# Kernel tuning notes

Measured on AMD Instinct MI355X. Metric: run time of the kernel, lower is better.

The kernel has to match this reference:

```python
import jax, jax.numpy as jnp
import numpy as np

WH, WW = 12, 12
NUM_HEADS = 8
NW = 4


def _relative_position_index():
    ch, cw = np.meshgrid(np.arange(WH), np.arange(WW), indexing='ij')
    coords = np.stack([ch, cw]).reshape(2, -1)            # [2, Wh*Ww]
    rel = coords[:, :, None] - coords[:, None, :]         # [2, M, M]
    rel = rel.transpose(1, 2, 0)                          # [M, M, 2]
    rel[:, :, 0] += WH - 1
    rel[:, :, 1] += WW - 1
    rel[:, :, 0] *= 2 * WW - 1
    return jnp.asarray(rel.sum(-1))                       # [M, M] int


def setup_inputs() -> dict:
    key = jax.random.key(0)
    ks = jax.random.split(key, 11)
    C = 512
    B_, N = 512, WH * WW + 1
    std = 0.02
    return {
        'x': jax.random.normal(ks[0], (B_, N, C), dtype=jnp.float32),
        'mask': jnp.zeros((NW, N, N), dtype=jnp.float32),
        'rpb_table': jax.random.normal(ks[1], ((2 * WH - 1) * (2 * WW - 1), NUM_HEADS), dtype=jnp.float32) * std,
        'Wq': jax.random.normal(ks[2], (C, C), dtype=jnp.float32) * (C ** -0.5),
        'bq': jax.random.normal(ks[3], (C,), dtype=jnp.float32) * std,
        'Wk': jax.random.normal(ks[4], (C, C), dtype=jnp.float32) * (C ** -0.5),
        'bk': jax.random.normal(ks[5], (C,), dtype=jnp.float32) * std,
        'Wv': jax.random.normal(ks[6], (C, C), dtype=jnp.float32) * (C ** -0.5),
        'bv': jax.random.normal(ks[7], (C,), dtype=jnp.float32) * std,
        'Wo': jax.random.normal(ks[8], (C, C), dtype=jnp.float32) * (C ** -0.5),
        'bo': jax.random.normal(ks[9], (C,), dtype=jnp.float32) * std,
    }


def reference(x, mask, rpb_table, Wq, bq, Wk, bk, Wv, bv, Wo, bo):
    B_, N, C = x.shape
    H = NUM_HEADS
    hd = C // H
    scale = hd ** -0.5
    B = B_ // NW
    M = WH * WW  # window tokens (N = M + 1 global token)

    def proj(W, b):
        return (x @ W.T + b).reshape(B_, N, H, hd).transpose(0, 2, 1, 3)  # [B_,H,N,hd]

    q = proj(Wq, bq)
    k = proj(Wk, bk)
    v = proj(Wv, bv)

    attn = jnp.einsum('bhnd,bhmd->bhnm', q, k) * scale  # [B_,H,N,N]

    rel_idx = _relative_position_index()                 # [M,M]
    bias = rpb_table[rel_idx].transpose(2, 0, 1)          # [H,M,M]
    attn = attn.at[:, :, :M, :M].add(bias[None])          # N != M: bias on window block only

    # shifted-window mask: (nW, N, N)
    attn = (attn.reshape(B, NW, H, N, N) + mask[None, :, None]).reshape(B_, H, N, N)

    # ---- global-token attention redistribution (gx) ----
    ga = attn[:, :, -1, :].reshape(B, NW, H, N).transpose(0, 2, 1, 3)   # [B,H,NW,N]
    g1 = ga[:, :, :, :M].reshape(B, H, NW * M)                           # window keys, all windows
    g2 = ga[:, :, :, M].mean(-1, keepdims=True)                          # mean global-global logit [B,H,1]
    g = jax.nn.softmax(jnp.concatenate([g1, g2], axis=-1), axis=-1)      # [B,H,NW*M+1]
    g1 = g[:, :, :-1].reshape(B, H, NW, M).transpose(0, 2, 1, 3).reshape(B_, H, M)
    g2 = jnp.broadcast_to(g[:, :, -1][:, None, :], (B, NW, H)).reshape(B_, H, 1)
    ga_full = jnp.concatenate([g1, g2], axis=-1)[:, :, None, :]          # [B_,H,1,N]
    gx = jnp.einsum('bhqn,bhnd->bhqd', ga_full, v).transpose(0, 2, 1, 3).reshape(B_, C)
    gx = gx.reshape(B, NW, C).sum(1)                                     # sum over windows [B,C]
    gx = jnp.broadcast_to(gx[:, None, :], (B, NW, C)).reshape(B_, C)

    # ---- standard window attention ----
    attn = jax.nn.softmax(attn, axis=-1)
    out = jnp.einsum('bhnm,bhmd->bhnd', attn, v).transpose(0, 2, 1, 3).reshape(B_, N, C)
    out = out.at[:, -1, :].set(gx)
    return out @ Wo.T + bo
```

## Files before the change

kernel.cpp:

```cpp
#include <hip/hip_runtime.h>
#include <hip/hip_bf16.h>
#include <stdint.h>

#define NTOK 145
#define MTOK 144
#define CDIM 512
#define NHEAD 8
#define HD 64
#define NWIN 4
#define BWIN 512
#define MROWS (BWIN*NTOK)

typedef short short8 __attribute__((ext_vector_type(8)));
typedef float f32x4 __attribute__((ext_vector_type(4)));

__device__ __forceinline__ uint16_t f2bf(float f) {
  union { float f; uint32_t u; } x; x.f = f;
  uint32_t r = x.u + 0x7FFFu + ((x.u >> 16) & 1u);
  return (uint16_t)(r >> 16);
}
__device__ __forceinline__ float bf2f(uint16_t u) {
  union { uint32_t u; float f; } x; x.u = ((uint32_t)u) << 16; return x.f;
}
__device__ __forceinline__ uint32_t pack2(float a, float b) {
  return (uint32_t)f2bf(a) | ((uint32_t)f2bf(b) << 16);
}

#define GLL(gp, lp) __builtin_amdgcn_global_load_lds( \
    (const __attribute__((address_space(1))) uint32_t*)(gp), \
    (__attribute__((address_space(3))) uint32_t*)(lp), 16, 0, 0)

__global__ __launch_bounds__(256) void cast_x(const float* __restrict__ x,
                                              uint16_t* __restrict__ xb) {
  size_t id = ((size_t)blockIdx.x*256 + threadIdx.x)*8;
  float4 a = *(const float4*)(x+id), c = *(const float4*)(x+id+4);
  uint4 o = make_uint4(pack2(a.x,a.y), pack2(a.z,a.w), pack2(c.x,c.y), pack2(c.z,c.w));
  *(uint4*)(xb+id) = o;
}

__global__ void prep_kernel(const float* __restrict__ rpb,
                            const float* __restrict__ Wq, const float* __restrict__ bq,
                            const float* __restrict__ Wk, const float* __restrict__ bk,
                            const float* __restrict__ Wv, const float* __restrict__ bv,
                            const float* __restrict__ Wo, const float* __restrict__ mask,
                            uint16_t* __restrict__ wqkv, uint16_t* __restrict__ wo,
                            float* __restrict__ bqkv, float* __restrict__ ltab) {
  int id = blockIdx.x * 256 + threadIdx.x;
  const int A = 1536*512, B = 512*512, C2 = 1536, E = 4*8*145*160;
  if (id < A) {
    int n = id >> 9, k = id & 511;
    const float* W = (n < 512) ? Wq : (n < 1024) ? Wk : Wv;
    wqkv[id] = f2bf(W[(size_t)(n & 511)*512 + k]);
  } else if ((id -= A) < B) {
    wo[id] = f2bf(Wo[id]);
  } else if ((id -= B) < C2) {
    bqkv[id] = (id < 512) ? bq[id] : (id < 1024) ? bk[id-512] : bv[id-1024];
  } else if ((id -= C2) < E) {
    int nw = id / (8*145*160);
    int r2 = id % (8*145*160);
    int h = r2 / (145*160);
    int r3 = r2 % (145*160);
    int i = r3 / 160, j = r3 % 160;
    float v = 0.f;
    if (j < 145) v = mask[(nw*145 + i)*145 + j];
    if (i < 144 && j < 144) {
      int rel = (i/12 - j/12 + 11) * 23 + (i%12 - j%12 + 11);
      v += rpb[rel*8 + h];
    }
    ltab[id] = v;
  }
}

__global__ __launch_bounds__(512, 2) void gemm_qkv(
    const uint16_t* __restrict__ xb, const uint16_t* __restrict__ wqkv,
    const float* __restrict__ bqkv,
    uint16_t* __restrict__ qb, uint16_t* __restrict__ kb, uint16_t* __restrict__ vb) {
  __shared__ __align__(16) uint16_t As[4*256*32];
  __shared__ __align__(16) uint16_t Bs[4*256*32];
  int bid = blockIdx.x;
  int mb, nb;
  if (bid < 1728) { int g = bid / 48, r = bid % 48; mb = g*8 + (r & 7); nb = r >> 3; }
  else            { int r = bid - 1728;             mb = 288 + (r & 1); nb = r >> 1; }
  int tid = threadIdx.x, lane = tid & 63, w = tid >> 6;
  int wnA = w >> 2;
  int wmB = w & 3;
  int lm = lane & 15, lq = lane >> 4;

  int srow = lane >> 2;
  int schunk = (lane & 3) ^ ((lane >> 3) & 3);
  const uint16_t* agp = xb   + (size_t)(mb*256 + w*32 + srow)*512 + schunk*8;
  const uint16_t* bgp = wqkv + (size_t)(nb*256 + w*32 + srow)*512 + schunk*8;
  int rc = (lq ^ ((lm >> 1) & 3)) * 8;

  f32x4 acc[8][4];
#pragma unroll
  for (int a = 0; a < 8; a++)
#pragma unroll
    for (int b = 0; b < 4; b++) acc[a][b] = (f32x4){0.f,0.f,0.f,0.f};

  #define STAGE_QKV(slot, kt) { \
    uint16_t* Ad = &As[(slot)*8192 + (w*32)*32]; \
    uint16_t* Bd = &Bs[(slot)*8192 + (w*32)*32]; \
    GLL(agp + (kt)*32,           Ad); \
    GLL(agp + (kt)*32 + 16*512,  Ad + 16*32); \
    GLL(bgp + (kt)*32,           Bd); \
    GLL(bgp + (kt)*32 + 16*512,  Bd + 16*32); \
  }

  #define COMPUTE_QKV(slot) { \
    const uint16_t* Wb = &Bs[(slot)*8192 + (wnA*128 + lm)*32 + rc]; \
    const uint16_t* Xb = &As[(slot)*8192 + (wmB*64  + lm)*32 + rc]; \
    short8 wf[8], xf[4]; \
    _Pragma("unroll") \
    for (int na = 0; na < 8; na++) wf[na] = *(const short8*)&Wb[na*16*32]; \
    _Pragma("unroll") \
    for (int mt = 0; mt < 4; mt++) xf[mt] = *(const short8*)&Xb[mt*16*32]; \
    __builtin_amdgcn_s_setprio(1); \
    _Pragma("unroll") \
    for (int na = 0; na < 8; na++) \
      _Pragma("unroll") \
      for (int mt = 0; mt < 4; mt++) \
        acc[na][mt] = __builtin_amdgcn_mfma_f32_16x16x32_bf16(wf[na], xf[mt], acc[na][mt], 0, 0, 0); \
    __builtin_amdgcn_s_setprio(0); \
  }

  STAGE_QKV(0, 0);
  STAGE_QKV(1, 1);
  for (int kt = 0; kt < 15; kt++) {
    asm volatile("s_waitcnt vmcnt(4)" ::: "memory");
    __builtin_amdgcn_s_barrier();
    __builtin_amdgcn_sched_barrier(0);
    if (kt < 14) STAGE_QKV((kt + 2) & 3, kt + 2);
    COMPUTE_QKV(kt & 3);
  }
  asm volatile("s_waitcnt vmcnt(0)" ::: "memory");
  __builtin_amdgcn_s_barrier();
  __builtin_amdgcn_sched_barrier(0);
  COMPUTE_QKV(3);

  #undef STAGE_QKV
  #undef COMPUTE_QKV

  int which = nb >> 1;
  uint16_t* dst = (which == 0) ? qb : (which == 1) ? kb : vb;
#pragma unroll
  for (int mt = 0; mt < 4; mt++) {
    int m = mb*256 + wmB*64 + mt*16 + lm;
    int bw = m / 145, nl = m - bw*145;
    size_t mbase = (size_t)bw*8*9280 + (size_t)nl*64;
#pragma unroll
    for (int na = 0; na < 8; na++) {
      int n0 = nb*256 + wnA*128 + na*16 + lq*4;
      float4 b4 = *(const float4*)&bqkv[n0];
      int c = n0 & 511;
      int hh = c >> 6, d0 = c & 63;
      float f0 = acc[na][mt][0] + b4.x;
      float f1 = acc[na][mt][1] + b4.y;
      float f2 = acc[na][mt][2] + b4.z;
      float f3 = acc[na][mt][3] + b4.w;
      uint32_t lo, hi;
      asm("v_cvt_pk_bf16_f32 %0, %1, %2" : "=v"(lo) : "v"(f0), "v"(f1));
      asm("v_cvt_pk_bf16_f32 %0, %1, %2" : "=v"(hi) : "v"(f2), "v"(f3));
      uint2 pk; pk.x = lo; pk.y = hi;
      *(uint2*)(dst + mbase + (size_t)hh*9280 + d0) = pk;
    }
  }
}

__global__ __launch_bounds__(256, 3) void attn_kernel(
    const uint16_t* __restrict__ qb, const uint16_t* __restrict__ kb,
    const uint16_t* __restrict__ vb, const float* __restrict__ ltab,
    float* __restrict__ glog, uint16_t* __restrict__ attn_out) {
  __shared__ __align__(16) uint16_t P[80*168];
  __shared__ __align__(16) uint16_t vt[64*168];
  int bid = blockIdx.x;
  int half = bid & 1;
  int h = (bid >> 1) & 7;
  int b_ = bid >> 4;
  int nw = b_ & 3;
  int tid = threadIdx.x, lane = tid & 63, w = tid >> 6;
  int lm = lane & 15, lq = lane >> 4;
  const size_t hbase = ((size_t)(b_*8 + h)) * (145*64);
  const uint16_t* qp = qb + hbase;
  const uint16_t* kp = kb + hbase;
  const uint16_t* vp = vb + hbase;
  const float* ltp = ltab + (size_t)(nw*8 + h)*(145*160);

  for (int c = tid; c < 1160; c += 256) {
    int j = c >> 3, d0 = (c & 7) * 8;
    uint16_t tmp[8];
    *(uint4*)tmp = *(const uint4*)(vp + (size_t)j*64 + d0);
#pragma unroll
    for (int t = 0; t < 8; t++) vt[(d0 + t)*168 + j] = tmp[t];
  }
  for (int c = tid; c < 960; c += 256)
    vt[(c/15)*168 + 145 + (c%15)] = 0;

  for (int ltile = w; ltile < 5; ltile += 4) {
    int gt = half*5 + ltile;
    f32x4 acc[10];
#pragma unroll
    for (int nt = 0; nt < 10; nt++) {
#pragma unroll
      for (int r = 0; r < 4; r++) {
        int i = gt*16 + lq*4 + r; if (i > 144) i = 144;
        acc[nt][r] = 8.0f * ltp[i*160 + nt*16 + lm];
      }
    }
    int iq = gt*16 + lm; if (iq > 144) iq = 144;
#pragma unroll
    for (int ks = 0; ks < 2; ks++) {
      short8 afr = *(const short8*)(qp + (size_t)iq*64 + ks*32 + lq*8);
#pragma unroll
      for (int nt = 0; nt < 10; nt++) {
        int j = nt*16 + lm; if (j > 144) j = 144;
        short8 bfr = *(const short8*)(kp + (size_t)j*64 + ks*32 + lq*8);
        acc[nt] = __builtin_amdgcn_mfma_f32_16x16x32_bf16(afr, bfr, acc[nt], 0, 0, 0);
      }
    }
    if (gt == 9) {
      if (lq == 0) {
#pragma unroll
        for (int nt = 0; nt < 10; nt++) {
          int j = nt*16 + lm;
          if (j < 145)
            glog[(size_t)(b_*8 + h)*145 + j] = acc[nt][0]*0.125f;
        }
      }
    } else {
#pragma unroll
      for (int r = 0; r < 4; r++) {
        int prow = ltile*16 + lq*4 + r;
        float mx = -3.0e38f;
#pragma unroll
        for (int nt = 0; nt < 10; nt++) {
          int j = nt*16 + lm;
          float t = acc[nt][r]*0.125f;
          if (j >= 145) t = -3.0e38f;
          acc[nt][r] = t;
          mx = fmaxf(mx, t);
        }
#pragma unroll
        for (int off = 1; off < 16; off <<= 1) mx = fmaxf(mx, __shfl_xor(mx, off));
        float sum = 0.f;
#pragma unroll
        for (int nt = 0; nt < 10; nt++) {
          int j = nt*16 + lm;
          float p = (j < 145) ? __expf(acc[nt][r] - mx) : 0.f;
          acc[nt][r] = p; sum += p;
        }
#pragma unroll
        for (int off = 1; off < 16; off <<= 1) sum += __shfl_xor(sum, off);
        float rs = __builtin_amdgcn_rcpf(sum);
#pragma unroll
        for (int nt = 0; nt < 10; nt++)
          P[prow*168 + nt*16 + lm] = f2bf(acc[nt][r] * rs);
      }
    }
  }
  __syncthreads();

  int npv = 5 - half;
  f32x4 oacc[5];
#pragma unroll
  for (int mt = 0; mt < 5; mt++) oacc[mt] = (f32x4){0.f,0.f,0.f,0.f};
#pragma unroll
  for (int ks = 0; ks < 5; ks++) {
    short8 bfr = *(const short8*)&vt[(w*16 + lm)*168 + ks*32 + lq*8];
#pragma unroll
    for (int mt = 0; mt < 5; mt++) {
      if (mt < npv) {
        short8 afr = *(const short8*)&P[(mt*16 + lm)*168 + ks*32 + lq*8];
        oacc[mt] = __builtin_amdgcn_mfma_f32_16x16x32_bf16(afr, bfr, oacc[mt], 0, 0, 0);
      }
    }
  }
#pragma unroll
  for (int mt = 0; mt < 5; mt++) {
    if (mt < npv) {
#pragma unroll
      for (int r = 0; r < 4; r++) {
        int i = half*80 + mt*16 + lq*4 + r;
        attn_out[((size_t)b_*145 + i)*512 + h*64 + w*16 + lm] = f2bf(oacc[mt][r]);
      }
    }
  }
}

__global__ __launch_bounds__(256) void gx_kernel(
    const float* __restrict__ glog, const uint16_t* __restrict__ vb,
    uint16_t* __restrict__ attn_out) {
  int bid = blockIdx.x;
  int b = bid >> 3, h = bid & 7;
  int tid = threadIdx.x, lane = tid & 63, w = tid >> 6;
  __shared__ float lg[580];
  __shared__ float pl[576];
  __shared__ float sred[8];
  __shared__ float sacc[256];
  for (int t = tid; t < 580; t += 256) {
    int nwi = t / 145, j = t - nwi*145;
    lg[t] = glog[(size_t)((b*4 + nwi)*8 + h)*145 + j];
  }
  __syncthreads();
  float g2 = 0.25f*(lg[144] + lg[289] + lg[434] + lg[579]);
  float mx = g2;
  for (int t = tid; t < 576; t += 256) {
    int nwi = t / 144, j = t - nwi*144;
    mx = fmaxf(mx, lg[nwi*145 + j]);
  }
#pragma unroll
  for (int off = 1; off < 64; off <<= 1) mx = fmaxf(mx, __shfl_xor(mx, off));
  if (lane == 0) sred[w] = mx;
  __syncthreads();
  mx = fmaxf(fmaxf(sred[0], sred[1]), fmaxf(sred[2], sred[3]));
  float sum = 0.f;
  for (int t = tid; t < 576; t += 256) {
    int nwi = t / 144, j = t - nwi*144;
    float p = __expf(lg[nwi*145 + j] - mx);
    pl[t] = p; sum += p;
  }
#pragma unroll
  for (int off = 1; off < 64; off <<= 1) sum += __shfl_xor(sum, off);
  if (lane == 0) sred[4 + w] = sum;
  __syncthreads();
  sum = (sred[4] + sred[5]) + (sred[6] + sred[7]);
  float p2 = __expf(g2 - mx);
  float rs = __builtin_amdgcn_rcpf(sum + p2);
  const uint16_t* vp = vb + (size_t)((b*4 + w)*8 + h)*(145*64);
  float acc = 0.f;
  int d = lane;
#pragma unroll 4
  for (int j = 0; j < 144; j++)
    acc += pl[w*144 + j] * bf2f(vp[j*64 + d]);
  acc += p2 * bf2f(vp[144*64 + d]);
  sacc[tid] = acc;
  __syncthreads();
  if (w == 0) {
    float tot = (sacc[lane] + sacc[64 + lane]) + (sacc[128 + lane] + sacc[192 + lane]);
    uint16_t o = f2bf(tot * rs);
    for (int nwi = 0; nwi < 4; nwi++)
      attn_out[((size_t)(b*4 + nwi)*145 + 144)*512 + h*64 + d] = o;
  }
}

__global__ __launch_bounds__(512, 2) void gemm_out(
    const uint16_t* __restrict__ A, const uint16_t* __restrict__ wo,
    const float* __restrict__ bo, float* __restrict__ out) {
  __shared__ __align__(16) uint16_t As[4*256*32];
  __shared__ __align__(16) uint16_t Bs[4*256*32];
  int bid = blockIdx.x;
  int mb, nb;
  if (bid < 576) { int g = bid / 16, r = bid % 16; mb = g*8 + (r & 7); nb = r >> 3; }
  else           { int r = bid - 576;              mb = 288 + (r & 1); nb = r >> 1; }
  int tid = threadIdx.x, lane = tid & 63, w = tid >> 6;
  int wnA = w >> 2;
  int wmB = w & 3;
  int lm = lane & 15, lq = lane >> 4;

  int srow = lane >> 2;
  int schunk = (lane & 3) ^ ((lane >> 3) & 3);
  const uint16_t* agp = A  + (size_t)(mb*256 + w*32 + srow)*512 + schunk*8;
  const uint16_t* bgp = wo + (size_t)(nb*256 + w*32 + srow)*512 + schunk*8;
  int rc = (lq ^ ((lm >> 1) & 3)) * 8;

  f32x4 acc[8][4];
#pragma unroll
  for (int a = 0; a < 8; a++)
#pragma unroll
    for (int b = 0; b < 4; b++) acc[a][b] = (f32x4){0.f,0.f,0.f,0.f};

  #define STAGE_O(slot, kt) { \
    uint16_t* Ad = &As[(slot)*8192 + (w*32)*32]; \
    uint16_t* Bd = &Bs[(slot)*8192 + (w*32)*32]; \
    GLL(agp + (kt)*32,           Ad); \
    GLL(agp + (kt)*32 + 16*512,  Ad + 16*32); \
    GLL(bgp + (kt)*32,           Bd); \
    GLL(bgp + (kt)*32 + 16*512,  Bd + 16*32); \
  }

  #define COMPUTE_O(slot) { \
    const uint16_t* Wb = &Bs[(slot)*8192 + (wnA*128 + lm)*32 + rc]; \
    const uint16_t* Xb = &As[(slot)*8192 + (wmB*64  + lm)*32 + rc]; \
    short8 wf[8], xf[4]; \
    _Pragma("unroll") \
    for (int na = 0; na < 8; na++) wf[na] = *(const short8*)&Wb[na*16*32]; \
    _Pragma("unroll") \
    for (int mt = 0; mt < 4; mt++) xf[mt] = *(const short8*)&Xb[mt*16*32]; \
    __builtin_amdgcn_s_setprio(1); \
    _Pragma("unroll") \
    for (int na = 0; na < 8; na++) \
      _Pragma("unroll") \
      for (int mt = 0; mt < 4; mt++) \
        acc[na][mt] = __builtin_amdgcn_mfma_f32_16x16x32_bf16(wf[na], xf[mt], acc[na][mt], 0, 0, 0); \
    __builtin_amdgcn_s_setprio(0); \
  }

  STAGE_O(0, 0);
  STAGE_O(1, 1);
  for (int kt = 0; kt < 15; kt++) {
    asm volatile("s_waitcnt vmcnt(4)" ::: "memory");
    __builtin_amdgcn_s_barrier();
    __builtin_amdgcn_sched_barrier(0);
    if (kt < 14) STAGE_O((kt + 2) & 3, kt + 2);
    COMPUTE_O(kt & 3);
  }
  asm volatile("s_waitcnt vmcnt(0)" ::: "memory");
  __builtin_amdgcn_s_barrier();
  __builtin_amdgcn_sched_barrier(0);
  COMPUTE_O(3);

  #undef STAGE_O
  #undef COMPUTE_O

#pragma unroll
  for (int mt = 0; mt < 4; mt++) {
    int m = mb*256 + wmB*64 + mt*16 + lm;
    float* orow = out + (size_t)m*512;
#pragma unroll
    for (int na = 0; na < 8; na++) {
      int n0 = nb*256 + wnA*128 + na*16 + lq*4;
      float4 b4 = *(const float4*)&bo[n0];
      float4 o;
      o.x = acc[na][mt][0] + b4.x;
      o.y = acc[na][mt][1] + b4.y;
      o.z = acc[na][mt][2] + b4.z;
      o.w = acc[na][mt][3] + b4.w;
      *(float4*)(orow + n0) = o;
    }
  }
}

extern "C" void kernel_launch(void* const* d_in, const int* in_sizes, int n_in,
                              void* d_out, int out_size, void* d_ws, size_t ws_size,
                              hipStream_t stream) {
  const float* x    = (const float*)d_in[0];
  const float* mask = (const float*)d_in[1];
  const float* rpb  = (const float*)d_in[2];
  const float* Wq   = (const float*)d_in[3];
  const float* bq   = (const float*)d_in[4];
  const float* Wk   = (const float*)d_in[5];
  const float* bk   = (const float*)d_in[6];
  const float* Wv   = (const float*)d_in[7];
  const float* bv   = (const float*)d_in[8];
  const float* Wo   = (const float*)d_in[9];
  const float* bo   = (const float*)d_in[10];

  uint8_t* ws = (uint8_t*)d_ws;
  size_t off = 0;
  auto alloc = [&](size_t bytes) -> void* {
    void* p = ws + off; off += (bytes + 255) & ~(size_t)255; return p;
  };
  uint16_t* wqkv   = (uint16_t*)alloc((size_t)1536*512*2);
  uint16_t* wo     = (uint16_t*)alloc((size_t)512*512*2);
  float*    bqkv   = (float*)alloc(1536*4);
  float*    ltab   = (float*)alloc((size_t)4*8*145*160*4);
  float*    glog   = (float*)alloc((size_t)512*8*145*4);
  uint16_t* xb     = (uint16_t*)alloc((size_t)MROWS*512*2);
  uint16_t* qb     = (uint16_t*)alloc((size_t)MROWS*512*2);
  uint16_t* kb     = (uint16_t*)alloc((size_t)MROWS*512*2);
  uint16_t* vb     = (uint16_t*)alloc((size_t)MROWS*512*2);
  uint16_t* attn   = (uint16_t*)alloc((size_t)MROWS*512*2);

  cast_x<<<18560, 256, 0, stream>>>(x, xb);
  prep_kernel<<<7002, 256, 0, stream>>>(rpb, Wq, bq, Wk, bk, Wv, bv, Wo, mask,
                                        wqkv, wo, bqkv, ltab);
  gemm_qkv<<<1740, 512, 0, stream>>>(xb, wqkv, bqkv, qb, kb, vb);
  attn_kernel<<<8192, 256, 0, stream>>>(qb, kb, vb, ltab, glog, attn);
  gx_kernel<<<1024, 256, 0, stream>>>(glog, vb, attn);
  gemm_out<<<580, 512, 0, stream>>>(attn, wo, bo, (float*)d_out);
}
```

Baseline: 720.1 us.

## Restructure attention kernel: one block per window-head, transposed QK, swizzled V LDS

```diff
diff --git a/kernel.cpp b/kernel.cpp
--- a/kernel.cpp
+++ b/kernel.cpp
@@ -44,9 +44,9 @@
                             const float* __restrict__ Wv, const float* __restrict__ bv,
                             const float* __restrict__ Wo, const float* __restrict__ mask,
                             uint16_t* __restrict__ wqkv, uint16_t* __restrict__ wo,
-                            float* __restrict__ bqkv, float* __restrict__ ltab) {
+                            float* __restrict__ bqkv, float* __restrict__ ltabT) {
   int id = blockIdx.x * 256 + threadIdx.x;
-  const int A = 1536*512, B = 512*512, C2 = 1536, E = 4*8*145*160;
+  const int A = 1536*512, B = 512*512, C2 = 1536, E = 4*8*160*160;
   if (id < A) {
     int n = id >> 9, k = id & 511;
     const float* W = (n < 512) ? Wq : (n < 1024) ? Wk : Wv;
@@ -56,18 +56,18 @@
   } else if ((id -= B) < C2) {
     bqkv[id] = (id < 512) ? bq[id] : (id < 1024) ? bk[id-512] : bv[id-1024];
   } else if ((id -= C2) < E) {
-    int nw = id / (8*145*160);
-    int r2 = id % (8*145*160);
-    int h = r2 / (145*160);
-    int r3 = r2 % (145*160);
-    int i = r3 / 160, j = r3 % 160;
+    int nw = id / 204800;
+    int r2 = id % 204800;
+    int h = r2 / 25600;
+    int r3 = r2 % 25600;
+    int j = r3 / 160, i = r3 % 160;
     float v = 0.f;
-    if (j < 145) v = mask[(nw*145 + i)*145 + j];
+    if (i < 145 && j < 145) v = mask[(nw*145 + i)*145 + j];
     if (i < 144 && j < 144) {
       int rel = (i/12 - j/12 + 11) * 23 + (i%12 - j%12 + 11);
       v += rpb[rel*8 + h];
     }
-    ltab[id] = v;
+    ltabT[id] = v;
   }
 }
 
@@ -167,123 +167,154 @@
   }
 }
 
-__global__ __launch_bounds__(256, 3) void attn_kernel(
+__global__ __launch_bounds__(320, 4) void attn_kernel(
     const uint16_t* __restrict__ qb, const uint16_t* __restrict__ kb,
-    const uint16_t* __restrict__ vb, const float* __restrict__ ltab,
+    const uint16_t* __restrict__ vb, const float* __restrict__ ltabT,
     float* __restrict__ glog, uint16_t* __restrict__ attn_out) {
-  __shared__ __align__(16) uint16_t P[80*168];
-  __shared__ __align__(16) uint16_t vt[64*168];
+  __shared__ __align__(16) uint16_t vt[64*192];
+  __shared__ __align__(16) uint16_t Pm[5*16*168];
   int bid = blockIdx.x;
-  int half = bid & 1;
-  int h = (bid >> 1) & 7;
-  int b_ = bid >> 4;
+  int b_ = bid >> 3, h = bid & 7;
   int nw = b_ & 3;
   int tid = threadIdx.x, lane = tid & 63, w = tid >> 6;
   int lm = lane & 15, lq = lane >> 4;
-  const size_t hbase = ((size_t)(b_*8 + h)) * (145*64);
+  const size_t hbase = ((size_t)bid) * (145*64);
   const uint16_t* qp = qb + hbase;
   const uint16_t* kp = kb + hbase;
   const uint16_t* vp = vb + hbase;
-  const float* ltp = ltab + (size_t)(nw*8 + h)*(145*160);
-
-  for (int c = tid; c < 1160; c += 256) {
+  const float* ltp = ltabT + (size_t)(nw*8 + h)*25600;
+  uint16_t* Pw = &Pm[w*16*168];
+
+  uint4 vval[4];
+#pragma unroll
+  for (int k = 0; k < 4; k++) {
+    int c = tid + k*320;
     int j = c >> 3, d0 = (c & 7) * 8;
-    uint16_t tmp[8];
-    *(uint4*)tmp = *(const uint4*)(vp + (size_t)j*64 + d0);
-#pragma unroll
-    for (int t = 0; t < 8; t++) vt[(d0 + t)*168 + j] = tmp[t];
-  }
-  for (int c = tid; c < 960; c += 256)
-    vt[(c/15)*168 + 145 + (c%15)] = 0;
-
-  for (int ltile = w; ltile < 5; ltile += 4) {
-    int gt = half*5 + ltile;
-    f32x4 acc[10];
-#pragma unroll
-    for (int nt = 0; nt < 10; nt++) {
-#pragma unroll
-      for (int r = 0; r < 4; r++) {
-        int i = gt*16 + lq*4 + r; if (i > 144) i = 144;
-        acc[nt][r] = 8.0f * ltp[i*160 + nt*16 + lm];
-      }
-    }
-    int iq = gt*16 + lm; if (iq > 144) iq = 144;
+    vval[k] = (j <= 144) ? *(const uint4*)(vp + (size_t)j*64 + d0)
+                         : make_uint4(0u,0u,0u,0u);
+  }
+
+  auto qk_tile = [&](int gt, f32x4* acc) {
+#pragma unroll
+    for (int nt = 0; nt < 10; nt++)
+#pragma unroll
+      for (int r = 0; r < 4; r++)
+        acc[nt][r] = 8.0f * ltp[(nt*16 + lq*4 + r)*160 + gt*16 + lm];
+    int i = gt*16 + lm; if (i > 144) i = 144;
 #pragma unroll
     for (int ks = 0; ks < 2; ks++) {
-      short8 afr = *(const short8*)(qp + (size_t)iq*64 + ks*32 + lq*8);
+      short8 qf = *(const short8*)(qp + (size_t)i*64 + ks*32 + lq*8);
 #pragma unroll
       for (int nt = 0; nt < 10; nt++) {
         int j = nt*16 + lm; if (j > 144) j = 144;
-        short8 bfr = *(const short8*)(kp + (size_t)j*64 + ks*32 + lq*8);
-        acc[nt] = __builtin_amdgcn_mfma_f32_16x16x32_bf16(afr, bfr, acc[nt], 0, 0, 0);
+        short8 kf = *(const short8*)(kp + (size_t)j*64 + ks*32 + lq*8);
+        acc[nt] = __builtin_amdgcn_mfma_f32_16x16x32_bf16(kf, qf, acc[nt], 0, 0, 0);
       }
     }
-    if (gt == 9) {
-      if (lq == 0) {
-#pragma unroll
-        for (int nt = 0; nt < 10; nt++) {
-          int j = nt*16 + lm;
-          if (j < 145)
-            glog[(size_t)(b_*8 + h)*145 + j] = acc[nt][0]*0.125f;
+  };
+
+  auto sm_store = [&](f32x4* acc) {
+    float mx = -3.0e38f;
+#pragma unroll
+    for (int nt = 0; nt < 10; nt++)
+#pragma unroll
+      for (int r = 0; r < 4; r++) {
+        int j = nt*16 + lq*4 + r;
+        float t = acc[nt][r]*0.125f;
+        if (j >= 145) t = -3.0e38f;
+        acc[nt][r] = t;
+        mx = fmaxf(mx, t);
+      }
+    mx = fmaxf(mx, __shfl_xor(mx, 16));
+    mx = fmaxf(mx, __shfl_xor(mx, 32));
+    float sum = 0.f;
+#pragma unroll
+    for (int nt = 0; nt < 10; nt++)
+#pragma unroll
+      for (int r = 0; r < 4; r++) {
+        int j = nt*16 + lq*4 + r;
+        float p = (j < 145) ? __expf(acc[nt][r] - mx) : 0.f;
+        acc[nt][r] = p; sum += p;
+      }
+    sum += __shfl_xor(sum, 16);
+    sum += __shfl_xor(sum, 32);
+    float rs = __builtin_amdgcn_rcpf(sum);
+#pragma unroll
+    for (int nt = 0; nt < 10; nt++) {
+      float f0 = acc[nt][0]*rs, f1 = acc[nt][1]*rs;
+      float f2 = acc[nt][2]*rs, f3 = acc[nt][3]*rs;
+      uint32_t lo, hi;
+      asm("v_cvt_pk_bf16_f32 %0, %1, %2" : "=v"(lo) : "v"(f0), "v"(f1));
+      asm("v_cvt_pk_bf16_f32 %0, %1, %2" : "=v"(hi) : "v"(f2), "v"(f3));
+      uint2 pk2; pk2.x = lo; pk2.y = hi;
+      *(uint2*)(Pw + lm*168 + nt*16 + lq*4) = pk2;
+    }
+  };
+
+  auto pv_tile = [&](int gt) {
+    short8 pa[5];
+#pragma unroll
+    for (int ks = 0; ks < 5; ks++)
+      pa[ks] = *(const short8*)(Pw + lm*168 + ks*32 + lq*8);
+#pragma unroll
+    for (int dq = 0; dq < 4; dq++) {
+      int d = dq*16 + lm;
+      int dswz = (d & 7) ^ ((d >> 3) & 7);
+      f32x4 o = (f32x4){0.f,0.f,0.f,0.f};
+#pragma unroll
+      for (int ks = 0; ks < 5; ks++) {
+        int chunk = (ks*4 + lq) ^ dswz;
+        short8 vf = *(const short8*)(vt + d*192 + chunk*8);
+        o = __builtin_amdgcn_mfma_f32_16x16x32_bf16(pa[ks], vf, o, 0, 0, 0);
+      }
+#pragma unroll
+      for (int r = 0; r < 4; r++) {
+        int i = gt*16 + lq*4 + r;
+        attn_out[((size_t)b_*145 + i)*512 + h*64 + d] = f2bf(o[r]);
+      }
+    }
+  };
+
+  {
+    f32x4 acc[10];
+    qk_tile(w, acc);
+    sm_store(acc);
+  }
+
+#pragma unroll
+  for (int k = 0; k < 4; k++) {
+    int c = tid + k*320;
+    int j = c >> 3;
+    uint16_t tmp[8];
+    *(uint4*)tmp = vval[k];
+#pragma unroll
+    for (int t = 0; t < 8; t++) {
+      int chunk = (j >> 3) ^ t ^ (c & 7);
+      vt[(8*(c & 7) + t)*192 + chunk*8 + (j & 7)] = tmp[t];
+    }
+  }
+  __syncthreads();
+
+  pv_tile(w);
+
+  if (w == 4) {
+    f32x4 acc[10];
+    qk_tile(9, acc);
+    if (lm == 0) {
+      size_t gb = (size_t)bid*145;
+#pragma unroll
+      for (int nt = 0; nt < 10; nt++)
+#pragma unroll
+        for (int r = 0; r < 4; r++) {
+          int j = nt*16 + lq*4 + r;
+          if (j < 145) glog[gb + j] = acc[nt][r]*0.125f;
         }
-      }
-    } else {
-#pragma unroll
-      for (int r = 0; r < 4; r++) {
-        int prow = ltile*16 + lq*4 + r;
-        float mx = -3.0e38f;
-#pragma unroll
-        for (int nt = 0; nt < 10; nt++) {
-          int j = nt*16 + lm;
-          float t = acc[nt][r]*0.125f;
-          if (j >= 145) t = -3.0e38f;
-          acc[nt][r] = t;
-          mx = fmaxf(mx, t);
-        }
-#pragma unroll
-        for (int off = 1; off < 16; off <<= 1) mx = fmaxf(mx, __shfl_xor(mx, off));
-        float sum = 0.f;
-#pragma unroll
-        for (int nt = 0; nt < 10; nt++) {
-          int j = nt*16 + lm;
-          float p = (j < 145) ? __expf(acc[nt][r] - mx) : 0.f;
-          acc[nt][r] = p; sum += p;
-        }
-#pragma unroll
-        for (int off = 1; off < 16; off <<= 1) sum += __shfl_xor(sum, off);
-        float rs = __builtin_amdgcn_rcpf(sum);
-#pragma unroll
-        for (int nt = 0; nt < 10; nt++)
-          P[prow*168 + nt*16 + lm] = f2bf(acc[nt][r] * rs);
-      }
-    }
-  }
-  __syncthreads();
-
-  int npv = 5 - half;
-  f32x4 oacc[5];
-#pragma unroll
-  for (int mt = 0; mt < 5; mt++) oacc[mt] = (f32x4){0.f,0.f,0.f,0.f};
-#pragma unroll
-  for (int ks = 0; ks < 5; ks++) {
-    short8 bfr = *(const short8*)&vt[(w*16 + lm)*168 + ks*32 + lq*8];
-#pragma unroll
-    for (int mt = 0; mt < 5; mt++) {
-      if (mt < npv) {
-        short8 afr = *(const short8*)&P[(mt*16 + lm)*168 + ks*32 + lq*8];
-        oacc[mt] = __builtin_amdgcn_mfma_f32_16x16x32_bf16(afr, bfr, oacc[mt], 0, 0, 0);
-      }
-    }
-  }
-#pragma unroll
-  for (int mt = 0; mt < 5; mt++) {
-    if (mt < npv) {
-#pragma unroll
-      for (int r = 0; r < 4; r++) {
-        int i = half*80 + mt*16 + lq*4 + r;
-        attn_out[((size_t)b_*145 + i)*512 + h*64 + w*16 + lm] = f2bf(oacc[mt][r]);
-      }
-    }
+    }
+  } else {
+    f32x4 acc[10];
+    qk_tile(w + 5, acc);
+    sm_store(acc);
+    pv_tile(w + 5);
   }
 }
 
@@ -453,7 +484,7 @@
   uint16_t* wqkv   = (uint16_t*)alloc((size_t)1536*512*2);
   uint16_t* wo     = (uint16_t*)alloc((size_t)512*512*2);
   float*    bqkv   = (float*)alloc(1536*4);
-  float*    ltab   = (float*)alloc((size_t)4*8*145*160*4);
+  float*    ltabT  = (float*)alloc((size_t)4*8*160*160*4);
   float*    glog   = (float*)alloc((size_t)512*8*145*4);
   uint16_t* xb     = (uint16_t*)alloc((size_t)MROWS*512*2);
   uint16_t* qb     = (uint16_t*)alloc((size_t)MROWS*512*2);
@@ -462,10 +493,10 @@
   uint16_t* attn   = (uint16_t*)alloc((size_t)MROWS*512*2);
 
   cast_x<<<18560, 256, 0, stream>>>(x, xb);
-  prep_kernel<<<7002, 256, 0, stream>>>(rpb, Wq, bq, Wk, bk, Wv, bv, Wo, mask,
-                                        wqkv, wo, bqkv, ltab);
+  prep_kernel<<<8102, 256, 0, stream>>>(rpb, Wq, bq, Wk, bk, Wv, bv, Wo, mask,
+                                        wqkv, wo, bqkv, ltabT);
   gemm_qkv<<<1740, 512, 0, stream>>>(xb, wqkv, bqkv, qb, kb, vb);
-  attn_kernel<<<8192, 256, 0, stream>>>(qb, kb, vb, ltab, glog, attn);
+  attn_kernel<<<4096, 320, 0, stream>>>(qb, kb, vb, ltabT, glog, attn);
   gx_kernel<<<1024, 256, 0, stream>>>(glog, vb, attn);
   gemm_out<<<580, 512, 0, stream>>>(attn, wo, bo, (float*)d_out);
 }
```

New measurement: 782.1 us. 1.09x slower.
